# Kernel tuning notes

Measured on AMD Instinct MI355X. Metric: run time of the kernel, lower is better.

The kernel has to match this reference:

```python
import jax, jax.numpy as jnp
import numpy as np

VDIM, HDIM, B = 128, 512, 512
EPS = 1e-5  # torch LayerNorm default


def _ln(x, g, b):
    m = x.mean(-1, keepdims=True)
    v = ((x - m) ** 2).mean(-1, keepdims=True)
    return (x - m) * jax.lax.rsqrt(v + EPS) * g + b


def setup_inputs() -> dict:
    key = jax.random.key(0)
    ks = jax.random.split(key, 16)
    s = 0.05  # small init so sigmoids/logs stay numerically tame
    d = {}
    d["u"] = jax.random.uniform(ks[0], (VDIM, B), jnp.float32)
    d["q_w1"] = s * jax.random.normal(ks[1], (VDIM, HDIM), jnp.float32)
    d["q_b1"] = jnp.zeros((HDIM,), jnp.float32)
    d["q_g1"] = jnp.ones((HDIM,), jnp.float32)
    d["q_be1"] = jnp.zeros((HDIM,), jnp.float32)
    d["q_w2"] = s * jax.random.normal(ks[2], (HDIM, HDIM), jnp.float32)
    d["q_b2"] = jnp.zeros((HDIM,), jnp.float32)
    d["q_g2"] = jnp.ones((HDIM,), jnp.float32)
    d["q_be2"] = jnp.zeros((HDIM,), jnp.float32)
    d["q_w3"] = s * jax.random.normal(ks[3], (HDIM, HDIM), jnp.float32)
    d["q_b3"] = jnp.zeros((HDIM,), jnp.float32)
    d["q_g3"] = jnp.ones((HDIM,), jnp.float32)
    d["q_be3"] = jnp.zeros((HDIM,), jnp.float32)
    d["q_W"] = 0.01 * jax.random.normal(ks[4], (VDIM, HDIM), jnp.float32)  # per-node output heads
    d["q_bias"] = jnp.zeros((VDIM,), jnp.float32)
    d["q_marg"] = jnp.zeros((VDIM,), jnp.float32)
    d["f_w1"] = s * jax.random.normal(ks[5], (VDIM, HDIM), jnp.float32)
    d["f_b1"] = jnp.zeros((HDIM,), jnp.float32)
    d["f_g1"] = jnp.ones((HDIM,), jnp.float32)
    d["f_be1"] = jnp.zeros((HDIM,), jnp.float32)
    d["f_w2"] = s * jax.random.normal(ks[6], (HDIM, HDIM), jnp.float32)
    d["f_b2"] = jnp.zeros((HDIM,), jnp.float32)
    d["f_g2"] = jnp.ones((HDIM,), jnp.float32)
    d["f_be2"] = jnp.zeros((HDIM,), jnp.float32)
    d["f_w3"] = s * jax.random.normal(ks[7], (HDIM, HDIM), jnp.float32)
    d["f_b3"] = jnp.zeros((HDIM,), jnp.float32)
    d["f_g3"] = jnp.ones((HDIM,), jnp.float32)
    d["f_be3"] = jnp.zeros((HDIM,), jnp.float32)
    d["f_w4"] = s * jax.random.normal(ks[8], (HDIM,), jnp.float32)
    d["f_b4"] = jnp.zeros((1,), jnp.float32)
    d["J"] = 0.1 * jax.random.normal(ks[9], (VDIM, VDIM), jnp.float32)  # Ising couplings for scorer
    d["top_order"] = jnp.arange(VDIM, dtype=jnp.int32)
    d["pa_mask"] = jax.random.randint(ks[10], (VDIM, VDIM), 0, 2, jnp.int32)
    return d


def reference(u, q_w1, q_b1, q_g1, q_be1, q_w2, q_b2, q_g2, q_be2,
              q_w3, q_b3, q_g3, q_be3, q_W, q_bias, q_marg,
              f_w1, f_b1, f_g1, f_be1, f_w2, f_b2, f_g2, f_be2,
              f_w3, f_b3, f_g3, f_be3, f_w4, f_b4, J,
              top_order, pa_mask):
    def qtrunk(V):
        h = jax.nn.relu(_ln(V @ q_w1 + q_b1, q_g1, q_be1))
        h = jax.nn.relu(_ln(h @ q_w2 + q_b2, q_g2, q_be2))
        h = jax.nn.relu(_ln(h @ q_w3 + q_b3, q_g3, q_be3))
        return h  # [B, H]

    def fnet(V):
        h = jax.nn.relu(_ln(V @ f_w1 + f_b1, f_g1, f_be1))
        h = jax.nn.relu(_ln(h @ f_w2 + f_b2, f_g2, f_be2))
        h = jax.nn.relu(_ln(h @ f_w3 + f_b3, f_g3, f_be3))
        return h @ f_w4 + f_b4[0]  # [B]

    # gather per-node quantities in topological order once, outside the scan
    masks = pa_mask[top_order].astype(u.dtype)          # [V, V] parent masks
    Wq = q_W[top_order]                                  # [V, H]
    bq = q_bias[top_order]                               # [V]
    mg = q_marg[top_order]                               # [V]
    oh = jax.nn.one_hot(top_order, VDIM, dtype=u.dtype)  # [V, V]

    def step(V, xs):
        mask_i, Wq_i, bq_i, mg_i, oh_i, u_i = xs
        V_pa = V * mask_i                                # [B, V] parents only
        x = qtrunk(V_pa) @ Wq_i + bq_i                   # [B]
        empty = jnp.abs(V_pa).sum(1) == 0
        p_on = jnp.where(empty, jax.nn.sigmoid(mg_i), jax.nn.sigmoid(x))
        samp = u_i < p_on                                # bernoulli(p_on)
        v_samp = 2.0 * samp.astype(u.dtype) - 1.0
        V_new = V * (1.0 - oh_i) + v_samp[:, None] * oh_i  # scatter into column
        lp = jnp.where(samp, jnp.log(p_on), jnp.log1p(-p_on))
        logF = fnet(jax.lax.stop_gradient(V_new))        # V.clone().detach()
        return V_new, (lp, logF)

    V0 = jnp.zeros((B, VDIM), u.dtype)
    V, (lps, logFs) = jax.lax.scan(step, V0, (masks, Wq, bq, mg, oh, u))
    log_pf = lps.T                                       # [B, V]
    F0 = fnet(V0)                                        # log_flow[:, 0] (alg='db')
    score = jax.lax.stop_gradient(jnp.einsum('bi,ij,bj->b', V, J, V))  # -energy, detached
    # last logF is overwritten by the terminal score, as in the original
    log_flow = jnp.concatenate([F0[:, None], logFs[:-1].T, score[:, None]], axis=1)  # [B, V+1]
    loss = ((log_flow[:, :-1] + log_pf - log_flow[:, 1:]) ** 2).mean(1).mean()
    return V, loss
```

## Files before the change

### kernel.cpp

```cpp
#include <hip/hip_runtime.h>
#include <hip/hip_bf16.h>
#include <math.h>

#define VDIM 128
#define HDIM 512
#define BATCH 512
#define RPB 4
#define NBLK (BATCH / RPB)
#define NT 512
#define LN_EPS 1e-5f
#define PF 4

#define FNT 256
#define FROWS 16
#define FRG (BATCH / FROWS)
#define FGRID (VDIM * FRG)

__device__ __forceinline__ float4 f4zero() { return make_float4(0.f, 0.f, 0.f, 0.f); }
__device__ __forceinline__ float4 f4add(float4 a, float4 b) {
    return make_float4(a.x + b.x, a.y + b.y, a.z + b.z, a.w + b.w);
}
__device__ __forceinline__ float4 f4fma(float4 a, float s, float4 c) {
    return make_float4(fmaf(a.x, s, c.x), fmaf(a.y, s, c.y),
                       fmaf(a.z, s, c.z), fmaf(a.w, s, c.w));
}
__device__ __forceinline__ float4 f4scale(float4 a, float s) {
    return make_float4(a.x * s, a.y * s, a.z * s, a.w * s);
}
__device__ __forceinline__ float4 f4sub(float4 a, float4 b) {
    return make_float4(a.x - b.x, a.y - b.y, a.z - b.z, a.w - b.w);
}
__device__ __forceinline__ float f4get(float4 v, int r) {
    return r == 0 ? v.x : r == 1 ? v.y : r == 2 ? v.z : v.w;
}

struct Params {
    const float *u;
    const float *q_w1, *q_b1, *q_g1, *q_be1;
    const float *q_w2, *q_b2, *q_g2, *q_be2;
    const float *q_w3, *q_b3, *q_g3, *q_be3;
    const float *q_W, *q_bias, *q_marg;
    const float *f_w1, *f_b1, *f_g1, *f_be1;
    const float *f_w2, *f_b2, *f_g2, *f_be2;
    const float *f_w3, *f_b3, *f_g3, *f_be3;
    const float *f_w4, *f_b4, *J;
    const int *top_order, *pa_mask;
    float *V_out, *lp, *lf, *score, *vs, *loss;
};

__device__ __forceinline__ float4 allreduce4(float4 v, float4 *red4, int tid) {
#pragma unroll
    for (int off = 1; off < 64; off <<= 1) {
        v.x += __shfl_xor(v.x, off, 64);
        v.y += __shfl_xor(v.y, off, 64);
        v.z += __shfl_xor(v.z, off, 64);
        v.w += __shfl_xor(v.w, off, 64);
    }
    if ((tid & 63) == 0) red4[tid >> 6] = v;
    __syncthreads();
    float4 s = red4[0];
#pragma unroll
    for (int w = 1; w < 8; ++w) s = f4add(s, red4[w]);
    __syncthreads();
    return s;
}

__device__ __forceinline__ float block_reduce1(float v, float *red, int tid) {
#pragma unroll
    for (int off = 1; off < 64; off <<= 1) v += __shfl_xor(v, off, 64);
    if ((tid & 63) == 0) red[tid >> 6] = v;
    __syncthreads();
    float s = 0.f;
#pragma unroll
    for (int w = 0; w < 8; ++w) s += red[w];
    __syncthreads();
    return s;
}

template <int K>
__device__ __forceinline__ void gemv_ln_scan(const float4 *__restrict__ inAT,
                                             const float *__restrict__ W,
                                             const float *__restrict__ bias,
                                             const float *__restrict__ gam,
                                             const float *__restrict__ bet,
                                             float4 *__restrict__ outAT,
                                             float4 (*partA)[8][64],
                                             float4 (*partB)[8][64],
                                             float4 *red4,
                                             int tid, int ks, int cq) {
    const int kc = K / 8;
    const float4 *inP = inAT + ks * kc;
    const float4 *Wk = (const float4 *)W + (size_t)(ks * kc) * (HDIM / 4) + cq;

    float4 acA0 = f4zero(), acA1 = f4zero(), acA2 = f4zero(), acA3 = f4zero();
    float4 acB0 = f4zero(), acB1 = f4zero(), acB2 = f4zero(), acB3 = f4zero();

    float4 wA[PF], wB[PF];
#pragma unroll
    for (int p = 0; p < PF; ++p) {
        wA[p] = Wk[(size_t)p * (HDIM / 4)];
        wB[p] = Wk[(size_t)p * (HDIM / 4) + 64];
    }
#pragma unroll 4
    for (int k = 0; k < kc - PF; ++k) {
        const int p = k & (PF - 1);
        float4 a = inP[k];
        float4 cA = wA[p], cB = wB[p];
        wA[p] = Wk[(size_t)(k + PF) * (HDIM / 4)];
        wB[p] = Wk[(size_t)(k + PF) * (HDIM / 4) + 64];
        acA0 = f4fma(a, cA.x, acA0); acA1 = f4fma(a, cA.y, acA1);
        acA2 = f4fma(a, cA.z, acA2); acA3 = f4fma(a, cA.w, acA3);
        acB0 = f4fma(a, cB.x, acB0); acB1 = f4fma(a, cB.y, acB1);
        acB2 = f4fma(a, cB.z, acB2); acB3 = f4fma(a, cB.w, acB3);
    }
#pragma unroll
    for (int k = kc - PF; k < kc; ++k) {
        const int p = k & (PF - 1);
        float4 a = inP[k];
        float4 cA = wA[p], cB = wB[p];
        acA0 = f4fma(a, cA.x, acA0); acA1 = f4fma(a, cA.y, acA1);
        acA2 = f4fma(a, cA.z, acA2); acA3 = f4fma(a, cA.w, acA3);
        acB0 = f4fma(a, cB.x, acB0); acB1 = f4fma(a, cB.y, acB1);
        acB2 = f4fma(a, cB.z, acB2); acB3 = f4fma(a, cB.w, acB3);
    }
    partA[0][ks][cq] = acA0; partA[1][ks][cq] = acA1;
    partA[2][ks][cq] = acA2; partA[3][ks][cq] = acA3;
    partB[0][ks][cq] = acB0; partB[1][ks][cq] = acB1;
    partB[2][ks][cq] = acB2; partB[3][ks][cq] = acB3;
    __syncthreads();

    const int jj = tid & 3;
    const int cc4 = (tid >> 2) & 63;
    float4 (*part)[8][64] = (tid < 256) ? partA : partB;
    float4 acc = part[jj][0][cc4];
#pragma unroll
    for (int s = 1; s < 8; ++s) acc = f4add(acc, part[jj][s][cc4]);
    float bc = bias[tid];
    acc.x += bc; acc.y += bc; acc.z += bc; acc.w += bc;

    const float inv = 1.f / (float)HDIM;
    float4 m4 = f4scale(allreduce4(acc, red4, tid), inv);
    float4 d = f4sub(acc, m4);
    float4 sq = make_float4(d.x * d.x, d.y * d.y, d.z * d.z, d.w * d.w);
    float4 var = f4scale(allreduce4(sq, red4, tid), inv);
    float4 rs;
    rs.x = 1.f / sqrtf(var.x + LN_EPS);
    rs.y = 1.f / sqrtf(var.y + LN_EPS);
    rs.z = 1.f / sqrtf(var.z + LN_EPS);
    rs.w = 1.f / sqrtf(var.w + LN_EPS);
    float gc = gam[tid], ec = bet[tid];
    float4 h;
    h.x = fmaxf(fmaf(d.x * rs.x, gc, ec), 0.f);
    h.y = fmaxf(fmaf(d.y * rs.y, gc, ec), 0.f);
    h.z = fmaxf(fmaf(d.z * rs.z, gc, ec), 0.f);
    h.w = fmaxf(fmaf(d.w * rs.w, gc, ec), 0.f);
    outAT[tid] = h;
    __syncthreads();
}

__global__ __launch_bounds__(NT) void gfn_scan(Params P) {
    __shared__ float4 VT[VDIM];
    __shared__ float4 VPT[VDIM];
    __shared__ float4 ATa[HDIM];
    __shared__ float4 ATb[HDIM];
    __shared__ float4 partA[4][8][64];
    __shared__ float4 partB[4][8][64];
    __shared__ float4 red4[8];

    const int tid = threadIdx.x;
    const int ks = tid >> 6;
    const int cq = tid & 63;
    const int row0 = blockIdx.x * RPB;

    if (tid < VDIM) VT[tid] = f4zero();
    __syncthreads();

    for (int i = 0; i < VDIM; ++i) {
        const int node = P.top_order[i];

        float4 ap = f4zero();
        if (tid < VDIM) {
            float mk = (float)P.pa_mask[node * VDIM + tid];
            float4 v = VT[tid];
            float4 vp = f4scale(v, mk);
            VPT[tid] = vp;
            ap = make_float4(fabsf(vp.x), fabsf(vp.y), fabsf(vp.z), fabsf(vp.w));
        }
        float4 asum = allreduce4(ap, red4, tid);

        gemv_ln_scan<VDIM>(VPT, P.q_w1, P.q_b1, P.q_g1, P.q_be1, ATa, partA, partB, red4, tid, ks, cq);
        gemv_ln_scan<HDIM>(ATa, P.q_w2, P.q_b2, P.q_g2, P.q_be2, ATb, partA, partB, red4, tid, ks, cq);
        gemv_ln_scan<HDIM>(ATb, P.q_w3, P.q_b3, P.q_g3, P.q_be3, ATa, partA, partB, red4, tid, ks, cq);

        float wq = P.q_W[(size_t)node * HDIM + tid];
        float4 xp = f4scale(ATa[tid], wq);
        float4 x4 = allreduce4(xp, red4, tid);

        if (tid < RPB) {
            const int r = tid;
            float asr = f4get(asum, r);
            float xr = f4get(x4, r) + P.q_bias[node];
            float arg = (asr == 0.f) ? P.q_marg[node] : xr;
            float p = 1.f / (1.f + expf(-arg));
            float uv = P.u[i * BATCH + row0 + r];
            bool samp = uv < p;
            float v = samp ? 1.f : -1.f;
            ((float *)&VT[node])[r] = v;
            P.vs[i * BATCH + row0 + r] = v;
            P.lp[i * BATCH + row0 + r] = samp ? logf(p) : log1pf(-p);
        }
        __syncthreads();
    }

    float4 inner = f4zero();
    if (tid < 128) {
#pragma unroll 4
        for (int ii = 0; ii < VDIM; ++ii)
            inner = f4fma(VT[ii], P.J[(size_t)ii * VDIM + tid], inner);
        float4 vc = VT[tid];
        inner = make_float4(inner.x * vc.x, inner.y * vc.y, inner.z * vc.z, inner.w * vc.w);
    }
    float4 sc4 = allreduce4(inner, red4, tid);
    if (tid < RPB) P.score[row0 + tid] = f4get(sc4, tid);
    if (tid < VDIM) {
        float4 v = VT[tid];
        P.V_out[(size_t)(row0 + 0) * VDIM + tid] = v.x;
        P.V_out[(size_t)(row0 + 1) * VDIM + tid] = v.y;
        P.V_out[(size_t)(row0 + 2) * VDIM + tid] = v.z;
        P.V_out[(size_t)(row0 + 3) * VDIM + tid] = v.w;
    }
}

__device__ __forceinline__ void reduce8_256(float4 &a, float4 &b,
                                            float4 *redA, float4 *redB, int tid) {
#pragma unroll
    for (int off = 1; off < 64; off <<= 1) {
        a.x += __shfl_xor(a.x, off, 64); a.y += __shfl_xor(a.y, off, 64);
        a.z += __shfl_xor(a.z, off, 64); a.w += __shfl_xor(a.w, off, 64);
        b.x += __shfl_xor(b.x, off, 64); b.y += __shfl_xor(b.y, off, 64);
        b.z += __shfl_xor(b.z, off, 64); b.w += __shfl_xor(b.w, off, 64);
    }
    int w = tid >> 6;
    if ((tid & 63) == 0) { redA[w] = a; redB[w] = b; }
    __syncthreads();
    int p = w ^ 1;
    a = f4add(redA[w], redA[p]);
    b = f4add(redB[w], redB[p]);
    __syncthreads();
}

template <int K>
__device__ __forceinline__ void flayer(const float *__restrict__ in,
                                       const float *__restrict__ W,
                                       const float *__restrict__ bias,
                                       const float *__restrict__ gam,
                                       const float *__restrict__ bet,
                                       float *__restrict__ out,
                                       float4 *redA, float4 *redB, int tid) {
    const int rh = tid >> 7, cq = tid & 127;
    const float4 *Wv = (const float4 *)W + cq;
    float4 accA[4], accB[4];
#pragma unroll
    for (int j = 0; j < 4; ++j) { accA[j] = f4zero(); accB[j] = f4zero(); }
#pragma unroll 4
    for (int k = 0; k < K; ++k) {
        float4 w = Wv[(size_t)k * (HDIM / 4)];
        const float *ip = in + k * FROWS + 8 * rh;
        float4 aA = *(const float4 *)ip;
        float4 aB = *(const float4 *)(ip + 4);
        accA[0] = f4fma(aA, w.x, accA[0]); accB[0] = f4fma(aB, w.x, accB[0]);
        accA[1] = f4fma(aA, w.y, accA[1]); accB[1] = f4fma(aB, w.y, accB[1]);
        accA[2] = f4fma(aA, w.z, accA[2]); accB[2] = f4fma(aB, w.z, accB[2]);
        accA[3] = f4fma(aA, w.w, accA[3]); accB[3] = f4fma(aB, w.w, accB[3]);
    }
    float4 b4 = ((const float4 *)bias)[cq];
    float bb[4] = {b4.x, b4.y, b4.z, b4.w};
#pragma unroll
    for (int j = 0; j < 4; ++j) {
        accA[j].x += bb[j]; accA[j].y += bb[j]; accA[j].z += bb[j]; accA[j].w += bb[j];
        accB[j].x += bb[j]; accB[j].y += bb[j]; accB[j].z += bb[j]; accB[j].w += bb[j];
    }
    const float inv = 1.f / (float)HDIM;
    float4 sA = f4add(f4add(accA[0], accA[1]), f4add(accA[2], accA[3]));
    float4 sB = f4add(f4add(accB[0], accB[1]), f4add(accB[2], accB[3]));
    reduce8_256(sA, sB, redA, redB, tid);
    float4 mA = f4scale(sA, inv), mB = f4scale(sB, inv);
    float4 dA[4], dB[4];
    float4 qA = f4zero(), qB = f4zero();
#pragma unroll
    for (int j = 0; j < 4; ++j) {
        dA[j] = f4sub(accA[j], mA);
        dB[j] = f4sub(accB[j], mB);
        qA.x += dA[j].x * dA[j].x; qA.y += dA[j].y * dA[j].y;
        qA.z += dA[j].z * dA[j].z; qA.w += dA[j].w * dA[j].w;
        qB.x += dB[j].x * dB[j].x; qB.y += dB[j].y * dB[j].y;
        qB.z += dB[j].z * dB[j].z; qB.w += dB[j].w * dB[j].w;
    }
    reduce8_256(qA, qB, redA, redB, tid);
    float4 rsA, rsB;
    rsA.x = 1.f / sqrtf(qA.x * inv + LN_EPS); rsA.y = 1.f / sqrtf(qA.y * inv + LN_EPS);
    rsA.z = 1.f / sqrtf(qA.z * inv + LN_EPS); rsA.w = 1.f / sqrtf(qA.w * inv + LN_EPS);
    rsB.x = 1.f / sqrtf(qB.x * inv + LN_EPS); rsB.y = 1.f / sqrtf(qB.y * inv + LN_EPS);
    rsB.z = 1.f / sqrtf(qB.z * inv + LN_EPS); rsB.w = 1.f / sqrtf(qB.w * inv + LN_EPS);
    float4 g4 = ((const float4 *)gam)[cq];
    float4 e4 = ((const float4 *)bet)[cq];
    float gg[4] = {g4.x, g4.y, g4.z, g4.w};
    float ee[4] = {e4.x, e4.y, e4.z, e4.w};
#pragma unroll
    for (int j = 0; j < 4; ++j) {
        float4 hA, hB;
        hA.x = fmaxf(fmaf(dA[j].x * rsA.x, gg[j], ee[j]), 0.f);
        hA.y = fmaxf(fmaf(dA[j].y * rsA.y, gg[j], ee[j]), 0.f);
        hA.z = fmaxf(fmaf(dA[j].z * rsA.z, gg[j], ee[j]), 0.f);
        hA.w = fmaxf(fmaf(dA[j].w * rsA.w, gg[j], ee[j]), 0.f);
        hB.x = fmaxf(fmaf(dB[j].x * rsB.x, gg[j], ee[j]), 0.f);
        hB.y = fmaxf(fmaf(dB[j].y * rsB.y, gg[j], ee[j]), 0.f);
        hB.z = fmaxf(fmaf(dB[j].z * rsB.z, gg[j], ee[j]), 0.f);
        hB.w = fmaxf(fmaf(dB[j].w * rsB.w, gg[j], ee[j]), 0.f);
        float *op = out + (4 * cq + j) * FROWS + 8 * rh;
        *(float4 *)op = hA;
        *(float4 *)(op + 4) = hB;
    }
    __syncthreads();
}

__global__ __launch_bounds__(FNT) void gfn_fnet(Params P) {
    __shared__ float Vt[VDIM * FROWS];
    __shared__ float A[HDIM * FROWS];
    __shared__ int ord[VDIM];
    __shared__ int invp[VDIM];
    __shared__ float4 redA[4], redB[4];

    const int tid = threadIdx.x;
    const int t = blockIdx.x >> 5;
    const int r0 = (blockIdx.x & 31) * FROWS;

    if (tid < VDIM) ord[tid] = P.top_order[tid];
    __syncthreads();
    if (tid < VDIM) invp[ord[tid]] = tid;
    __syncthreads();
    for (int idx = tid; idx < VDIM * FROWS; idx += FNT) {
        int k = idx >> 4, row = idx & 15;
        int s = invp[k];
        Vt[idx] = (s <= t) ? P.vs[s * BATCH + r0 + row] : 0.f;
    }
    __syncthreads();

    flayer<VDIM>(Vt, P.f_w1, P.f_b1, P.f_g1, P.f_be1, A, redA, redB, tid);
    flayer<HDIM>(A, P.f_w2, P.f_b2, P.f_g2, P.f_be2, A, redA, redB, tid);
    flayer<HDIM>(A, P.f_w3, P.f_b3, P.f_g3, P.f_be3, A, redA, redB, tid);

    const int rh = tid >> 7, cq = tid & 127;
    float4 w4 = ((const float4 *)P.f_w4)[cq];
    float ww[4] = {w4.x, w4.y, w4.z, w4.w};
    float4 sA = f4zero(), sB = f4zero();
#pragma unroll
    for (int j = 0; j < 4; ++j) {
        const float *ap = A + (4 * cq + j) * FROWS + 8 * rh;
        float4 aA = *(const float4 *)ap;
        float4 aB = *(const float4 *)(ap + 4);
        sA = f4fma(aA, ww[j], sA);
        sB = f4fma(aB, ww[j], sB);
    }
    reduce8_256(sA, sB, redA, redB, tid);
    if (cq == 0) {
        float b4v = P.f_b4[0];
        float *dst = P.lf + (size_t)t * BATCH + r0 + 8 * rh;
        dst[0] = sA.x + b4v; dst[1] = sA.y + b4v;
        dst[2] = sA.z + b4v; dst[3] = sA.w + b4v;
        dst[4] = sB.x + b4v; dst[5] = sB.y + b4v;
        dst[6] = sB.z + b4v; dst[7] = sB.w + b4v;
    }
}

__global__ __launch_bounds__(NT) void gfn_loss(Params P) {
    __shared__ float H1[HDIM], H2[HDIM];
    __shared__ float red1[8];
    const int tid = threadIdx.x;
    const float inv = 1.f / (float)HDIM;

    float z = P.f_b1[tid];
    float m = block_reduce1(z, red1, tid) * inv;
    float d = z - m;
    float var = block_reduce1(d * d, red1, tid) * inv;
    float h = fmaxf(fmaf(d * (1.f / sqrtf(var + LN_EPS)), P.f_g1[tid], P.f_be1[tid]), 0.f);
    H1[tid] = h;
    __syncthreads();

    float acc = 0.f;
    for (int k = 0; k < HDIM; ++k) acc = fmaf(H1[k], P.f_w2[(size_t)k * HDIM + tid], acc);
    z = acc + P.f_b2[tid];
    m = block_reduce1(z, red1, tid) * inv;
    d = z - m;
    var = block_reduce1(d * d, red1, tid) * inv;
    h = fmaxf(fmaf(d * (1.f / sqrtf(var + LN_EPS)), P.f_g2[tid], P.f_be2[tid]), 0.f);
    H2[tid] = h;
    __syncthreads();

    acc = 0.f;
    for (int k = 0; k < HDIM; ++k) acc = fmaf(H2[k], P.f_w3[(size_t)k * HDIM + tid], acc);
    z = acc + P.f_b3[tid];
    m = block_reduce1(z, red1, tid) * inv;
    d = z - m;
    var = block_reduce1(d * d, red1, tid) * inv;
    h = fmaxf(fmaf(d * (1.f / sqrtf(var + LN_EPS)), P.f_g3[tid], P.f_be3[tid]), 0.f);
    float F0 = block_reduce1(h * P.f_w4[tid], red1, tid) + P.f_b4[0];

    const int b = tid;
    float lfp = F0;
    float s = 0.f;
    for (int t = 0; t < VDIM; ++t) {
        float lp = P.lp[t * BATCH + b];
        float lfn = (t == VDIM - 1) ? P.score[b] : P.lf[t * BATCH + b];
        float dd = lfp + lp - lfn;
        s = fmaf(dd, dd, s);
        lfp = lfn;
    }
    s *= (1.f / (float)VDIM);
    float total = block_reduce1(s, red1, tid) * (1.f / (float)BATCH);
    if (tid == 0) P.loss[0] = total;
}

extern "C" void kernel_launch(void *const *d_in, const int *in_sizes, int n_in,
                              void *d_out, int out_size, void *d_ws, size_t ws_size,
                              hipStream_t stream) {
    Params P;
    P.u     = (const float *)d_in[0];
    P.q_w1  = (const float *)d_in[1];
    P.q_b1  = (const float *)d_in[2];
    P.q_g1  = (const float *)d_in[3];
    P.q_be1 = (const float *)d_in[4];
    P.q_w2  = (const float *)d_in[5];
    P.q_b2  = (const float *)d_in[6];
    P.q_g2  = (const float *)d_in[7];
    P.q_be2 = (const float *)d_in[8];
    P.q_w3  = (const float *)d_in[9];
    P.q_b3  = (const float *)d_in[10];
    P.q_g3  = (const float *)d_in[11];
    P.q_be3 = (const float *)d_in[12];
    P.q_W   = (const float *)d_in[13];
    P.q_bias= (const float *)d_in[14];
    P.q_marg= (const float *)d_in[15];
    P.f_w1  = (const float *)d_in[16];
    P.f_b1  = (const float *)d_in[17];
    P.f_g1  = (const float *)d_in[18];
    P.f_be1 = (const float *)d_in[19];
    P.f_w2  = (const float *)d_in[20];
    P.f_b2  = (const float *)d_in[21];
    P.f_g2  = (const float *)d_in[22];
    P.f_be2 = (const float *)d_in[23];
    P.f_w3  = (const float *)d_in[24];
    P.f_b3  = (const float *)d_in[25];
    P.f_g3  = (const float *)d_in[26];
    P.f_be3 = (const float *)d_in[27];
    P.f_w4  = (const float *)d_in[28];
    P.f_b4  = (const float *)d_in[29];
    P.J     = (const float *)d_in[30];
    P.top_order = (const int *)d_in[31];
    P.pa_mask   = (const int *)d_in[32];

    float *ws = (float *)d_ws;
    P.V_out = (float *)d_out;
    P.loss  = (float *)d_out + (size_t)BATCH * VDIM;
    P.lp    = ws;
    P.lf    = ws + (size_t)VDIM * BATCH;
    P.score = ws + 2 * (size_t)VDIM * BATCH;
    P.vs    = ws + 2 * (size_t)VDIM * BATCH + BATCH;

    gfn_scan<<<dim3(NBLK), dim3(NT), 0, stream>>>(P);
    gfn_fnet<<<dim3(FGRID), dim3(FNT), 0, stream>>>(P);
    gfn_loss<<<dim3(1), dim3(NT), 0, stream>>>(P);
}
```

Baseline: 4.705 ms.

## Fuse scan and flow-net kernels into one persistent launch with flag-based overlap

Merges the sequential scan kernel and the flow-net evaluation kernel into a single launch. 128 blocks run the scan while 128 worker blocks compute the flow-net tiles as soon as per-block progress flags show that step t is done, so the two phases overlap. It also changes the scan GEMV split from 8 k-slices to 4, with 128-column quads per thread, and widens flow-net tiles to 32 rows. The cost is spin-waiting on global atomics and threadfence overhead. It also relies on all 256 blocks being co-resident, otherwise the workers can deadlock.

```diff
diff --git a/kernel.cpp b/kernel.cpp
--- a/kernel.cpp
+++ b/kernel.cpp
@@ -7,14 +7,13 @@
 #define BATCH 512
 #define RPB 4
 #define NBLK (BATCH / RPB)
+#define NWORK 128
 #define NT 512
+#define NWAVE 8
 #define LN_EPS 1e-5f
-#define PF 4
-
-#define FNT 256
-#define FROWS 16
-#define FRG (BATCH / FROWS)
-#define FGRID (VDIM * FRG)
+#define FROWS 32
+#define NGRP (BATCH / FROWS)
+#define SBPG (FROWS / RPB)
 
 __device__ __forceinline__ float4 f4zero() { return make_float4(0.f, 0.f, 0.f, 0.f); }
 __device__ __forceinline__ float4 f4add(float4 a, float4 b) {
@@ -45,10 +44,27 @@
     const float *f_w3, *f_b3, *f_g3, *f_be3;
     const float *f_w4, *f_b4, *J;
     const int *top_order, *pa_mask;
+    int *flag;
     float *V_out, *lp, *lf, *score, *vs, *loss;
 };
 
-__device__ __forceinline__ float4 allreduce4(float4 v, float4 *red4, int tid) {
+struct ScanS {
+    float4 VT[VDIM];
+    float4 VPT[VDIM];
+    float4 ATa[HDIM];
+    float4 ATb[HDIM];
+    float4 part[4][4][128];
+    float4 redA[NWAVE], redB[NWAVE];
+};
+struct WorkS {
+    float Vt[VDIM * FROWS];
+    float A[HDIM * FROWS];
+    int ord[VDIM], invp[VDIM];
+    float4 redA[NWAVE], redB[NWAVE];
+};
+union SMem { ScanS s; WorkS w; };
+
+__device__ __forceinline__ float4 allreduce4_1s(float4 v, float4 *red, int tid) {
 #pragma unroll
     for (int off = 1; off < 64; off <<= 1) {
         v.x += __shfl_xor(v.x, off, 64);
@@ -56,12 +72,11 @@
         v.z += __shfl_xor(v.z, off, 64);
         v.w += __shfl_xor(v.w, off, 64);
     }
-    if ((tid & 63) == 0) red4[tid >> 6] = v;
-    __syncthreads();
-    float4 s = red4[0];
-#pragma unroll
-    for (int w = 1; w < 8; ++w) s = f4add(s, red4[w]);
-    __syncthreads();
+    if ((tid & 63) == 0) red[tid >> 6] = v;
+    __syncthreads();
+    float4 s = red[0];
+#pragma unroll
+    for (int w = 1; w < NWAVE; ++w) s = f4add(s, red[w]);
     return s;
 }
 
@@ -72,129 +87,121 @@
     __syncthreads();
     float s = 0.f;
 #pragma unroll
-    for (int w = 0; w < 8; ++w) s += red[w];
+    for (int w = 0; w < NWAVE; ++w) s += red[w];
     __syncthreads();
     return s;
 }
 
+__device__ __forceinline__ void redpair(float4 &a, float4 &b,
+                                        float4 *redA, float4 *redB, int tid) {
+#pragma unroll
+    for (int off = 1; off < 64; off <<= 1) {
+        a.x += __shfl_xor(a.x, off, 64); a.y += __shfl_xor(a.y, off, 64);
+        a.z += __shfl_xor(a.z, off, 64); a.w += __shfl_xor(a.w, off, 64);
+        b.x += __shfl_xor(b.x, off, 64); b.y += __shfl_xor(b.y, off, 64);
+        b.z += __shfl_xor(b.z, off, 64); b.w += __shfl_xor(b.w, off, 64);
+    }
+    int w = tid >> 6;
+    if ((tid & 63) == 0) { redA[w] = a; redB[w] = b; }
+    __syncthreads();
+    int p = w ^ 1;
+    a = f4add(redA[w], redA[p]);
+    b = f4add(redB[w], redB[p]);
+    __syncthreads();
+}
+
 template <int K>
-__device__ __forceinline__ void gemv_ln_scan(const float4 *__restrict__ inAT,
+__device__ __forceinline__ void gemv_ln_scan(const float4 *__restrict__ inA,
                                              const float *__restrict__ W,
                                              const float *__restrict__ bias,
                                              const float *__restrict__ gam,
                                              const float *__restrict__ bet,
-                                             float4 *__restrict__ outAT,
-                                             float4 (*partA)[8][64],
-                                             float4 (*partB)[8][64],
-                                             float4 *red4,
-                                             int tid, int ks, int cq) {
-    const int kc = K / 8;
-    const float4 *inP = inAT + ks * kc;
-    const float4 *Wk = (const float4 *)W + (size_t)(ks * kc) * (HDIM / 4) + cq;
-
-    float4 acA0 = f4zero(), acA1 = f4zero(), acA2 = f4zero(), acA3 = f4zero();
-    float4 acB0 = f4zero(), acB1 = f4zero(), acB2 = f4zero(), acB3 = f4zero();
-
-    float4 wA[PF], wB[PF];
-#pragma unroll
-    for (int p = 0; p < PF; ++p) {
-        wA[p] = Wk[(size_t)p * (HDIM / 4)];
-        wB[p] = Wk[(size_t)p * (HDIM / 4) + 64];
-    }
-#pragma unroll 4
-    for (int k = 0; k < kc - PF; ++k) {
-        const int p = k & (PF - 1);
-        float4 a = inP[k];
-        float4 cA = wA[p], cB = wB[p];
-        wA[p] = Wk[(size_t)(k + PF) * (HDIM / 4)];
-        wB[p] = Wk[(size_t)(k + PF) * (HDIM / 4) + 64];
-        acA0 = f4fma(a, cA.x, acA0); acA1 = f4fma(a, cA.y, acA1);
-        acA2 = f4fma(a, cA.z, acA2); acA3 = f4fma(a, cA.w, acA3);
-        acB0 = f4fma(a, cB.x, acB0); acB1 = f4fma(a, cB.y, acB1);
-        acB2 = f4fma(a, cB.z, acB2); acB3 = f4fma(a, cB.w, acB3);
-    }
-#pragma unroll
-    for (int k = kc - PF; k < kc; ++k) {
-        const int p = k & (PF - 1);
-        float4 a = inP[k];
-        float4 cA = wA[p], cB = wB[p];
-        acA0 = f4fma(a, cA.x, acA0); acA1 = f4fma(a, cA.y, acA1);
-        acA2 = f4fma(a, cA.z, acA2); acA3 = f4fma(a, cA.w, acA3);
-        acB0 = f4fma(a, cB.x, acB0); acB1 = f4fma(a, cB.y, acB1);
-        acB2 = f4fma(a, cB.z, acB2); acB3 = f4fma(a, cB.w, acB3);
-    }
-    partA[0][ks][cq] = acA0; partA[1][ks][cq] = acA1;
-    partA[2][ks][cq] = acA2; partA[3][ks][cq] = acA3;
-    partB[0][ks][cq] = acB0; partB[1][ks][cq] = acB1;
-    partB[2][ks][cq] = acB2; partB[3][ks][cq] = acB3;
-    __syncthreads();
-
-    const int jj = tid & 3;
-    const int cc4 = (tid >> 2) & 63;
-    float4 (*part)[8][64] = (tid < 256) ? partA : partB;
-    float4 acc = part[jj][0][cc4];
-#pragma unroll
-    for (int s = 1; s < 8; ++s) acc = f4add(acc, part[jj][s][cc4]);
-    float bc = bias[tid];
+                                             float4 *__restrict__ outA,
+                                             ScanS &S, int tid, int ks, int cq,
+                                             int myc) {
+    constexpr int kc = K / 4;
+    constexpr int q4 = kc / 4;
+    constexpr int seg = K / 4;
+    const float4 *Wp = (const float4 *)W + (size_t)(ks * kc) * (HDIM / 4) + cq;
+    const float4 *ap = inA + ks * q4;
+    float4 acc0 = f4zero(), acc1 = f4zero(), acc2 = f4zero(), acc3 = f4zero();
+#pragma unroll 2
+    for (int q = 0; q < q4; ++q) {
+        float4 a0 = ap[q];
+        float4 a1 = ap[q + seg];
+        float4 a2 = ap[q + 2 * seg];
+        float4 a3 = ap[q + 3 * seg];
+        float4 w0 = Wp[(size_t)(4 * q + 0) * (HDIM / 4)];
+        float4 w1 = Wp[(size_t)(4 * q + 1) * (HDIM / 4)];
+        float4 w2 = Wp[(size_t)(4 * q + 2) * (HDIM / 4)];
+        float4 w3 = Wp[(size_t)(4 * q + 3) * (HDIM / 4)];
+        acc0 = f4fma(a0, w0.x, acc0); acc1 = f4fma(a0, w0.y, acc1);
+        acc2 = f4fma(a0, w0.z, acc2); acc3 = f4fma(a0, w0.w, acc3);
+        acc0 = f4fma(a1, w1.x, acc0); acc1 = f4fma(a1, w1.y, acc1);
+        acc2 = f4fma(a1, w1.z, acc2); acc3 = f4fma(a1, w1.w, acc3);
+        acc0 = f4fma(a2, w2.x, acc0); acc1 = f4fma(a2, w2.y, acc1);
+        acc2 = f4fma(a2, w2.z, acc2); acc3 = f4fma(a2, w2.w, acc3);
+        acc0 = f4fma(a3, w3.x, acc0); acc1 = f4fma(a3, w3.y, acc1);
+        acc2 = f4fma(a3, w3.z, acc2); acc3 = f4fma(a3, w3.w, acc3);
+    }
+    S.part[0][ks][cq] = acc0;
+    S.part[1][ks][cq] = acc1;
+    S.part[2][ks][cq] = acc2;
+    S.part[3][ks][cq] = acc3;
+    __syncthreads();
+    const int j = ks, cb = cq;
+    float4 acc = f4add(f4add(S.part[j][0][cb], S.part[j][1][cb]),
+                       f4add(S.part[j][2][cb], S.part[j][3][cb]));
+    float bc = bias[myc];
     acc.x += bc; acc.y += bc; acc.z += bc; acc.w += bc;
-
     const float inv = 1.f / (float)HDIM;
-    float4 m4 = f4scale(allreduce4(acc, red4, tid), inv);
+    float4 m4 = f4scale(allreduce4_1s(acc, S.redA, tid), inv);
     float4 d = f4sub(acc, m4);
     float4 sq = make_float4(d.x * d.x, d.y * d.y, d.z * d.z, d.w * d.w);
-    float4 var = f4scale(allreduce4(sq, red4, tid), inv);
+    float4 var = f4scale(allreduce4_1s(sq, S.redB, tid), inv);
     float4 rs;
     rs.x = 1.f / sqrtf(var.x + LN_EPS);
     rs.y = 1.f / sqrtf(var.y + LN_EPS);
     rs.z = 1.f / sqrtf(var.z + LN_EPS);
     rs.w = 1.f / sqrtf(var.w + LN_EPS);
-    float gc = gam[tid], ec = bet[tid];
+    float gc = gam[myc], ec = bet[myc];
     float4 h;
     h.x = fmaxf(fmaf(d.x * rs.x, gc, ec), 0.f);
     h.y = fmaxf(fmaf(d.y * rs.y, gc, ec), 0.f);
     h.z = fmaxf(fmaf(d.z * rs.z, gc, ec), 0.f);
     h.w = fmaxf(fmaf(d.w * rs.w, gc, ec), 0.f);
-    outAT[tid] = h;
-    __syncthreads();
-}
-
-__global__ __launch_bounds__(NT) void gfn_scan(Params P) {
-    __shared__ float4 VT[VDIM];
-    __shared__ float4 VPT[VDIM];
-    __shared__ float4 ATa[HDIM];
-    __shared__ float4 ATb[HDIM];
-    __shared__ float4 partA[4][8][64];
-    __shared__ float4 partB[4][8][64];
-    __shared__ float4 red4[8];
-
+    outA[tid] = h;
+    __syncthreads();
+}
+
+__device__ void scan_role(const Params &P, int bid, ScanS &S) {
     const int tid = threadIdx.x;
-    const int ks = tid >> 6;
-    const int cq = tid & 63;
-    const int row0 = blockIdx.x * RPB;
-
-    if (tid < VDIM) VT[tid] = f4zero();
+    const int ks = tid >> 7;
+    const int cq = tid & 127;
+    const int myc = 4 * cq + ks;
+    const int row0 = bid * RPB;
+
+    if (tid < VDIM) S.VT[tid] = f4zero();
     __syncthreads();
 
     for (int i = 0; i < VDIM; ++i) {
         const int node = P.top_order[i];
 
-        float4 ap = f4zero();
+        float4 apv = f4zero();
         if (tid < VDIM) {
             float mk = (float)P.pa_mask[node * VDIM + tid];
-            float4 v = VT[tid];
-            float4 vp = f4scale(v, mk);
-            VPT[tid] = vp;
-            ap = make_float4(fabsf(vp.x), fabsf(vp.y), fabsf(vp.z), fabsf(vp.w));
-        }
-        float4 asum = allreduce4(ap, red4, tid);
-
-        gemv_ln_scan<VDIM>(VPT, P.q_w1, P.q_b1, P.q_g1, P.q_be1, ATa, partA, partB, red4, tid, ks, cq);
-        gemv_ln_scan<HDIM>(ATa, P.q_w2, P.q_b2, P.q_g2, P.q_be2, ATb, partA, partB, red4, tid, ks, cq);
-        gemv_ln_scan<HDIM>(ATb, P.q_w3, P.q_b3, P.q_g3, P.q_be3, ATa, partA, partB, red4, tid, ks, cq);
-
-        float wq = P.q_W[(size_t)node * HDIM + tid];
-        float4 xp = f4scale(ATa[tid], wq);
-        float4 x4 = allreduce4(xp, red4, tid);
+            float4 vp = f4scale(S.VT[tid], mk);
+            S.VPT[(tid & 3) * 32 + (tid >> 2)] = vp;
+            apv = make_float4(fabsf(vp.x), fabsf(vp.y), fabsf(vp.z), fabsf(vp.w));
+        }
+        float4 asum = allreduce4_1s(apv, S.redB, tid);
+
+        gemv_ln_scan<VDIM>(S.VPT, P.q_w1, P.q_b1, P.q_g1, P.q_be1, S.ATa, S, tid, ks, cq, myc);
+        gemv_ln_scan<HDIM>(S.ATa, P.q_w2, P.q_b2, P.q_g2, P.q_be2, S.ATb, S, tid, ks, cq, myc);
+        gemv_ln_scan<HDIM>(S.ATb, P.q_w3, P.q_b3, P.q_g3, P.q_be3, S.ATa, S, tid, ks, cq, myc);
+
+        float wq = P.q_W[(size_t)node * HDIM + myc];
+        float4 x4 = allreduce4_1s(f4scale(S.ATa[tid], wq), S.redA, tid);
 
         if (tid < RPB) {
             const int r = tid;
@@ -205,25 +212,27 @@
             float uv = P.u[i * BATCH + row0 + r];
             bool samp = uv < p;
             float v = samp ? 1.f : -1.f;
-            ((float *)&VT[node])[r] = v;
-            P.vs[i * BATCH + row0 + r] = v;
-            P.lp[i * BATCH + row0 + r] = samp ? logf(p) : log1pf(-p);
+            ((float *)&S.VT[node])[r] = v;
+            P.vs[(size_t)i * BATCH + row0 + r] = v;
+            P.lp[(size_t)i * BATCH + row0 + r] = samp ? logf(p) : log1pf(-p);
+            __threadfence();
         }
         __syncthreads();
+        if (tid == 0) atomicExch(P.flag + bid, i + 1);
     }
 
     float4 inner = f4zero();
-    if (tid < 128) {
+    if (tid < VDIM) {
 #pragma unroll 4
         for (int ii = 0; ii < VDIM; ++ii)
-            inner = f4fma(VT[ii], P.J[(size_t)ii * VDIM + tid], inner);
-        float4 vc = VT[tid];
+            inner = f4fma(S.VT[ii], P.J[(size_t)ii * VDIM + tid], inner);
+        float4 vc = S.VT[tid];
         inner = make_float4(inner.x * vc.x, inner.y * vc.y, inner.z * vc.z, inner.w * vc.w);
     }
-    float4 sc4 = allreduce4(inner, red4, tid);
+    float4 sc4 = allreduce4_1s(inner, S.redA, tid);
     if (tid < RPB) P.score[row0 + tid] = f4get(sc4, tid);
     if (tid < VDIM) {
-        float4 v = VT[tid];
+        float4 v = S.VT[tid];
         P.V_out[(size_t)(row0 + 0) * VDIM + tid] = v.x;
         P.V_out[(size_t)(row0 + 1) * VDIM + tid] = v.y;
         P.V_out[(size_t)(row0 + 2) * VDIM + tid] = v.z;
@@ -231,33 +240,16 @@
     }
 }
 
-__device__ __forceinline__ void reduce8_256(float4 &a, float4 &b,
-                                            float4 *redA, float4 *redB, int tid) {
-#pragma unroll
-    for (int off = 1; off < 64; off <<= 1) {
-        a.x += __shfl_xor(a.x, off, 64); a.y += __shfl_xor(a.y, off, 64);
-        a.z += __shfl_xor(a.z, off, 64); a.w += __shfl_xor(a.w, off, 64);
-        b.x += __shfl_xor(b.x, off, 64); b.y += __shfl_xor(b.y, off, 64);
-        b.z += __shfl_xor(b.z, off, 64); b.w += __shfl_xor(b.w, off, 64);
-    }
-    int w = tid >> 6;
-    if ((tid & 63) == 0) { redA[w] = a; redB[w] = b; }
-    __syncthreads();
-    int p = w ^ 1;
-    a = f4add(redA[w], redA[p]);
-    b = f4add(redB[w], redB[p]);
-    __syncthreads();
-}
-
 template <int K>
-__device__ __forceinline__ void flayer(const float *__restrict__ in,
-                                       const float *__restrict__ W,
-                                       const float *__restrict__ bias,
-                                       const float *__restrict__ gam,
-                                       const float *__restrict__ bet,
-                                       float *__restrict__ out,
-                                       float4 *redA, float4 *redB, int tid) {
-    const int rh = tid >> 7, cq = tid & 127;
+__device__ __forceinline__ void flayer512(const float *__restrict__ in,
+                                          const float *__restrict__ W,
+                                          const float *__restrict__ bias,
+                                          const float *__restrict__ gam,
+                                          const float *__restrict__ bet,
+                                          float *__restrict__ out,
+                                          float4 *redA, float4 *redB, int tid) {
+    const int rh = tid >> 7;
+    const int cq = tid & 127;
     const float4 *Wv = (const float4 *)W + cq;
     float4 accA[4], accB[4];
 #pragma unroll
@@ -266,12 +258,12 @@
     for (int k = 0; k < K; ++k) {
         float4 w = Wv[(size_t)k * (HDIM / 4)];
         const float *ip = in + k * FROWS + 8 * rh;
-        float4 aA = *(const float4 *)ip;
-        float4 aB = *(const float4 *)(ip + 4);
-        accA[0] = f4fma(aA, w.x, accA[0]); accB[0] = f4fma(aB, w.x, accB[0]);
-        accA[1] = f4fma(aA, w.y, accA[1]); accB[1] = f4fma(aB, w.y, accB[1]);
-        accA[2] = f4fma(aA, w.z, accA[2]); accB[2] = f4fma(aB, w.z, accB[2]);
-        accA[3] = f4fma(aA, w.w, accA[3]); accB[3] = f4fma(aB, w.w, accB[3]);
+        float4 vA = *(const float4 *)ip;
+        float4 vB = *(const float4 *)(ip + 4);
+        accA[0] = f4fma(vA, w.x, accA[0]); accB[0] = f4fma(vB, w.x, accB[0]);
+        accA[1] = f4fma(vA, w.y, accA[1]); accB[1] = f4fma(vB, w.y, accB[1]);
+        accA[2] = f4fma(vA, w.z, accA[2]); accB[2] = f4fma(vB, w.z, accB[2]);
+        accA[3] = f4fma(vA, w.w, accA[3]); accB[3] = f4fma(vB, w.w, accB[3]);
     }
     float4 b4 = ((const float4 *)bias)[cq];
     float bb[4] = {b4.x, b4.y, b4.z, b4.w};
@@ -283,7 +275,7 @@
     const float inv = 1.f / (float)HDIM;
     float4 sA = f4add(f4add(accA[0], accA[1]), f4add(accA[2], accA[3]));
     float4 sB = f4add(f4add(accB[0], accB[1]), f4add(accB[2], accB[3]));
-    reduce8_256(sA, sB, redA, redB, tid);
+    redpair(sA, sB, redA, redB, tid);
     float4 mA = f4scale(sA, inv), mB = f4scale(sB, inv);
     float4 dA[4], dB[4];
     float4 qA = f4zero(), qB = f4zero();
@@ -296,7 +288,7 @@
         qB.x += dB[j].x * dB[j].x; qB.y += dB[j].y * dB[j].y;
         qB.z += dB[j].z * dB[j].z; qB.w += dB[j].w * dB[j].w;
     }
-    reduce8_256(qA, qB, redA, redB, tid);
+    redpair(qA, qB, redA, redB, tid);
     float4 rsA, rsB;
     rsA.x = 1.f / sqrtf(qA.x * inv + LN_EPS); rsA.y = 1.f / sqrtf(qA.y * inv + LN_EPS);
     rsA.z = 1.f / sqrtf(qA.z * inv + LN_EPS); rsA.w = 1.f / sqrtf(qA.w * inv + LN_EPS);
@@ -324,58 +316,72 @@
     __syncthreads();
 }
 
-__global__ __launch_bounds__(FNT) void gfn_fnet(Params P) {
-    __shared__ float Vt[VDIM * FROWS];
-    __shared__ float A[HDIM * FROWS];
-    __shared__ int ord[VDIM];
-    __shared__ int invp[VDIM];
-    __shared__ float4 redA[4], redB[4];
-
+__device__ void worker_role(const Params &P, int wid, WorkS &S) {
     const int tid = threadIdx.x;
-    const int t = blockIdx.x >> 5;
-    const int r0 = (blockIdx.x & 31) * FROWS;
-
-    if (tid < VDIM) ord[tid] = P.top_order[tid];
-    __syncthreads();
-    if (tid < VDIM) invp[ord[tid]] = tid;
-    __syncthreads();
-    for (int idx = tid; idx < VDIM * FROWS; idx += FNT) {
-        int k = idx >> 4, row = idx & 15;
-        int s = invp[k];
-        Vt[idx] = (s <= t) ? P.vs[s * BATCH + r0 + row] : 0.f;
-    }
-    __syncthreads();
-
-    flayer<VDIM>(Vt, P.f_w1, P.f_b1, P.f_g1, P.f_be1, A, redA, redB, tid);
-    flayer<HDIM>(A, P.f_w2, P.f_b2, P.f_g2, P.f_be2, A, redA, redB, tid);
-    flayer<HDIM>(A, P.f_w3, P.f_b3, P.f_g3, P.f_be3, A, redA, redB, tid);
-
-    const int rh = tid >> 7, cq = tid & 127;
-    float4 w4 = ((const float4 *)P.f_w4)[cq];
-    float ww[4] = {w4.x, w4.y, w4.z, w4.w};
-    float4 sA = f4zero(), sB = f4zero();
-#pragma unroll
-    for (int j = 0; j < 4; ++j) {
-        const float *ap = A + (4 * cq + j) * FROWS + 8 * rh;
-        float4 aA = *(const float4 *)ap;
-        float4 aB = *(const float4 *)(ap + 4);
-        sA = f4fma(aA, ww[j], sA);
-        sB = f4fma(aB, ww[j], sB);
-    }
-    reduce8_256(sA, sB, redA, redB, tid);
-    if (cq == 0) {
-        float b4v = P.f_b4[0];
-        float *dst = P.lf + (size_t)t * BATCH + r0 + 8 * rh;
-        dst[0] = sA.x + b4v; dst[1] = sA.y + b4v;
-        dst[2] = sA.z + b4v; dst[3] = sA.w + b4v;
-        dst[4] = sB.x + b4v; dst[5] = sB.y + b4v;
-        dst[6] = sB.z + b4v; dst[7] = sB.w + b4v;
-    }
+    if (tid < VDIM) S.ord[tid] = P.top_order[tid];
+    __syncthreads();
+    if (tid < VDIM) S.invp[S.ord[tid]] = tid;
+    __syncthreads();
+    const int g = wid & (NGRP - 1);
+    const int r0 = g * FROWS;
+
+    for (int tile = wid; tile < VDIM * NGRP; tile += NWORK) {
+        const int t = tile >> 4;
+        if (t == VDIM - 1) continue;
+        if (tid == 0) {
+            const int need = t + 1;
+            for (int b = 0; b < SBPG; ++b) {
+                while (atomicAdd(P.flag + (SBPG * g + b), 0) < need)
+                    __builtin_amdgcn_s_sleep(8);
+            }
+            __threadfence();
+        }
+        __syncthreads();
+        for (int idx = tid; idx < VDIM * FROWS; idx += NT) {
+            int k = idx >> 5, rr = idx & (FROWS - 1);
+            int s = S.invp[k];
+            S.Vt[idx] = (s <= t) ? P.vs[(size_t)s * BATCH + r0 + rr] : 0.f;
+        }
+        __syncthreads();
+
+        flayer512<VDIM>(S.Vt, P.f_w1, P.f_b1, P.f_g1, P.f_be1, S.A, S.redA, S.redB, tid);
+        flayer512<HDIM>(S.A, P.f_w2, P.f_b2, P.f_g2, P.f_be2, S.A, S.redA, S.redB, tid);
+        flayer512<HDIM>(S.A, P.f_w3, P.f_b3, P.f_g3, P.f_be3, S.A, S.redA, S.redB, tid);
+
+        const int rh = tid >> 7, cq = tid & 127;
+        float4 w4 = ((const float4 *)P.f_w4)[cq];
+        float ww[4] = {w4.x, w4.y, w4.z, w4.w};
+        float4 sA = f4zero(), sB = f4zero();
+#pragma unroll
+        for (int j = 0; j < 4; ++j) {
+            const float *ap2 = S.A + (4 * cq + j) * FROWS + 8 * rh;
+            float4 vA = *(const float4 *)ap2;
+            float4 vB = *(const float4 *)(ap2 + 4);
+            sA = f4fma(vA, ww[j], sA);
+            sB = f4fma(vB, ww[j], sB);
+        }
+        redpair(sA, sB, S.redA, S.redB, tid);
+        if (cq == 0) {
+            float b4v = P.f_b4[0];
+            float *dst = P.lf + (size_t)t * BATCH + r0 + 8 * rh;
+            dst[0] = sA.x + b4v; dst[1] = sA.y + b4v;
+            dst[2] = sA.z + b4v; dst[3] = sA.w + b4v;
+            dst[4] = sB.x + b4v; dst[5] = sB.y + b4v;
+            dst[6] = sB.z + b4v; dst[7] = sB.w + b4v;
+        }
+        __syncthreads();
+    }
+}
+
+__global__ __launch_bounds__(NT) void gfn_main(Params P) {
+    __shared__ SMem sm;
+    if (blockIdx.x < NBLK) scan_role(P, blockIdx.x, sm.s);
+    else                   worker_role(P, blockIdx.x - NBLK, sm.w);
 }
 
 __global__ __launch_bounds__(NT) void gfn_loss(Params P) {
     __shared__ float H1[HDIM], H2[HDIM];
-    __shared__ float red1[8];
+    __shared__ float red1[NWAVE];
     const int tid = threadIdx.x;
     const float inv = 1.f / (float)HDIM;
 
@@ -410,8 +416,8 @@
     float lfp = F0;
     float s = 0.f;
     for (int t = 0; t < VDIM; ++t) {
-        float lp = P.lp[t * BATCH + b];
-        float lfn = (t == VDIM - 1) ? P.score[b] : P.lf[t * BATCH + b];
+        float lp = P.lp[(size_t)t * BATCH + b];
+        float lfn = (t == VDIM - 1) ? P.score[b] : P.lf[(size_t)t * BATCH + b];
         float dd = lfp + lp - lfn;
         s = fmaf(dd, dd, s);
         lfp = lfn;
@@ -466,8 +472,9 @@
     P.lf    = ws + (size_t)VDIM * BATCH;
     P.score = ws + 2 * (size_t)VDIM * BATCH;
     P.vs    = ws + 2 * (size_t)VDIM * BATCH + BATCH;
-
-    gfn_scan<<<dim3(NBLK), dim3(NT), 0, stream>>>(P);
-    gfn_fnet<<<dim3(FGRID), dim3(FNT), 0, stream>>>(P);
+    P.flag  = (int *)(ws + 3 * (size_t)VDIM * BATCH + BATCH);
+
+    hipMemsetAsync(P.flag, 0, NBLK * sizeof(int), stream);
+    gfn_main<<<dim3(NBLK + NWORK), dim3(NT), 0, stream>>>(P);
     gfn_loss<<<dim3(1), dim3(NT), 0, stream>>>(P);
 }
```

New measurement: 4.344 ms. -7.7%, faster.
